# Optimization experiments

Measured on AMD Instinct MI355X. Metric: run time of the kernel, lower is better.

The kernel has to match this reference:

```python
import jax, jax.numpy as jnp
import numpy as np


def squash(t, axis=-1):
    sq = jnp.sum(t * t, axis=axis, keepdims=True)
    scale = sq / (1.0 + sq)
    return scale * t / jnp.sqrt(sq + 1e-8)


def setup_inputs() -> dict:
    key = jax.random.key(0)
    k1, k2 = jax.random.split(key)
    B, in_caps, out_caps, in_dim, out_dim = 128, 2048, 32, 8, 16
    x = jax.random.normal(k1, (B, in_caps, in_dim), dtype=jnp.float32)
    W = jax.random.normal(k2, (in_caps, out_caps, in_dim, out_dim), dtype=jnp.float32)
    return {"x": x, "W": W}


def reference(x, W):
    # x: [B, in_caps, in_dim], W: [in_caps, out_caps, in_dim, out_dim]
    # u_hat: [B, in_caps, out_caps, out_dim]
    u_hat = jnp.einsum('bni,noid->bnod', x, W)
    B, in_caps, out_caps, _ = u_hat.shape
    b = jnp.zeros((B, in_caps, out_caps, 1), dtype=u_hat.dtype)
    v = None
    for i in range(3):
        c = jax.nn.softmax(b, axis=2)              # over out_caps
        s = jnp.sum(c * u_hat, axis=1)             # [B, out_caps, out_dim]
        v = squash(s)                              # [B, out_caps, out_dim]
        if i < 2:
            b = b + jnp.sum(u_hat * v[:, None], axis=-1, keepdims=True)
    return v
```

## Files before the change

### kernel.cpp

```cpp
#include <hip/hip_runtime.h>


constexpr int NC = 2048;
constexpr int OC = 32;
constexpr int OD = 16;

typedef const __attribute__((address_space(1))) void* gas1_t;
typedef __attribute__((address_space(3))) void* las3_t;

__device__ __forceinline__ void gld16(const void* g, void* l) {
    __builtin_amdgcn_global_load_lds((gas1_t)g, (las3_t)l, 16, 0, 0);
}

#define MEMFENCE() asm volatile("" ::: "memory")
#define BAR() do { MEMFENCE(); __builtin_amdgcn_s_barrier(); MEMFENCE(); } while (0)

template<int NR, bool FIRST, bool ATOMIC>
__global__ __launch_bounds__(256)
void caps_pass(const float* __restrict__ xg, const float* __restrict__ Wg,
               const float* __restrict__ vin, float* __restrict__ pout)
{
    __shared__ float4 Wl[2][1024];

    constexpr int NSUPC = 2048 / NR;
    const int tid  = threadIdx.x;
    const int bid  = blockIdx.x;
    const int bt   = bid / NSUPC;
    const int nsup = bid % NSUPC;
    const int w    = __builtin_amdgcn_readfirstlane(tid >> 6);
    const int lane = tid & 63;
    const int o    = lane & 31;
    const int h    = lane >> 5;
    const int sw   = o & 7;
    const int b0   = bt * 16 + w * 4;
    const int nbase = nsup * NR;

    const float4* Wg4 = (const float4*)Wg;

    float4 acc[4][2];
#pragma unroll
    for (int r = 0; r < 4; ++r)
#pragma unroll
        for (int qq = 0; qq < 2; ++qq) acc[r][qq] = make_float4(0.f, 0.f, 0.f, 0.f);

    float4 vr[4][2];
    if (!FIRST) {
        const float4* v4 = (const float4*)vin;
#pragma unroll
        for (int r = 0; r < 4; ++r)
#pragma unroll
            for (int qq = 0; qq < 2; ++qq)
                vr[r][qq] = v4[(size_t)(b0 + r) * 128 + o * 4 + h * 2 + qq];
    }

#pragma unroll
    for (int j = 0; j < 4; ++j) {
        const int L = tid + 256 * j;
        const int oo = L >> 5, cc = L & 31;
        gld16(&Wg4[(size_t)nbase * 1024 + oo * 32 + (cc ^ (oo & 7))], &Wl[0][L]);
    }

#pragma unroll 1
    for (int t = 0; t < NR; ++t) {
        BAR();
        if (t + 1 < NR) {
#pragma unroll
            for (int j = 0; j < 4; ++j) {
                const int L = tid + 256 * j;
                const int oo = L >> 5, cc = L & 31;
                gld16(&Wg4[(size_t)(nbase + t + 1) * 1024 + oo * 32 + (cc ^ (oo & 7))],
                      &Wl[(t + 1) & 1][L]);
            }
            asm volatile("s_waitcnt vmcnt(4)" ::: "memory");
        } else {
            asm volatile("s_waitcnt vmcnt(0)" ::: "memory");
        }
        BAR();

        const int n = nbase + t;
        float xs[4][8];
#pragma unroll
        for (int r = 0; r < 4; ++r) {
            const float* xp = xg + ((size_t)(b0 + r) * NC + n) * 8;
#pragma unroll
            for (int i = 0; i < 8; ++i) xs[r][i] = xp[i];
        }
        const float4* wrow = &Wl[t & 1][o * 32];

        __builtin_amdgcn_s_setprio(1);
        if (FIRST) {
#pragma unroll
            for (int i = 0; i < 8; ++i)
#pragma unroll
                for (int qq = 0; qq < 2; ++qq) {
                    const float4 wv = wrow[(i * 4 + h * 2 + qq) ^ sw];
#pragma unroll
                    for (int r = 0; r < 4; ++r) {
                        acc[r][qq].x = fmaf(xs[r][i], wv.x, acc[r][qq].x);
                        acc[r][qq].y = fmaf(xs[r][i], wv.y, acc[r][qq].y);
                        acc[r][qq].z = fmaf(xs[r][i], wv.z, acc[r][qq].z);
                        acc[r][qq].w = fmaf(xs[r][i], wv.w, acc[r][qq].w);
                    }
                }
        } else {
            float4 u[4][2];
#pragma unroll
            for (int r = 0; r < 4; ++r)
#pragma unroll
                for (int qq = 0; qq < 2; ++qq) u[r][qq] = make_float4(0.f, 0.f, 0.f, 0.f);
#pragma unroll
            for (int i = 0; i < 8; ++i)
#pragma unroll
                for (int qq = 0; qq < 2; ++qq) {
                    const float4 wv = wrow[(i * 4 + h * 2 + qq) ^ sw];
#pragma unroll
                    for (int r = 0; r < 4; ++r) {
                        u[r][qq].x = fmaf(xs[r][i], wv.x, u[r][qq].x);
                        u[r][qq].y = fmaf(xs[r][i], wv.y, u[r][qq].y);
                        u[r][qq].z = fmaf(xs[r][i], wv.z, u[r][qq].z);
                        u[r][qq].w = fmaf(xs[r][i], wv.w, u[r][qq].w);
                    }
                }
#pragma unroll
            for (int r = 0; r < 4; ++r) {
                float tp = 0.f;
#pragma unroll
                for (int qq = 0; qq < 2; ++qq) {
                    tp = fmaf(u[r][qq].x, vr[r][qq].x, tp);
                    tp = fmaf(u[r][qq].y, vr[r][qq].y, tp);
                    tp = fmaf(u[r][qq].z, vr[r][qq].z, tp);
                    tp = fmaf(u[r][qq].w, vr[r][qq].w, tp);
                }
                const float tt = tp + __shfl_xor(tp, 32);
                const float e = __expf(tt);
                float Z = e;
                Z += __shfl_xor(Z, 1);
                Z += __shfl_xor(Z, 2);
                Z += __shfl_xor(Z, 4);
                Z += __shfl_xor(Z, 8);
                Z += __shfl_xor(Z, 16);
                const float c = e / Z;
#pragma unroll
                for (int qq = 0; qq < 2; ++qq) {
                    acc[r][qq].x = fmaf(c, u[r][qq].x, acc[r][qq].x);
                    acc[r][qq].y = fmaf(c, u[r][qq].y, acc[r][qq].y);
                    acc[r][qq].z = fmaf(c, u[r][qq].z, acc[r][qq].z);
                    acc[r][qq].w = fmaf(c, u[r][qq].w, acc[r][qq].w);
                }
            }
        }
        __builtin_amdgcn_s_setprio(0);
    }

    const float sc = FIRST ? (1.0f / 32.0f) : 1.0f;
    if (ATOMIC) {
#pragma unroll
        for (int r = 0; r < 4; ++r) {
            float* sb = pout + (size_t)(b0 + r) * (OC * OD) + o * OD + h * 8;
#pragma unroll
            for (int qq = 0; qq < 2; ++qq) {
                atomicAdd(sb + qq * 4 + 0, acc[r][qq].x * sc);
                atomicAdd(sb + qq * 4 + 1, acc[r][qq].y * sc);
                atomicAdd(sb + qq * 4 + 2, acc[r][qq].z * sc);
                atomicAdd(sb + qq * 4 + 3, acc[r][qq].w * sc);
            }
        }
    } else {
        float4* P4 = (float4*)pout;
#pragma unroll
        for (int r = 0; r < 4; ++r) {
            const size_t base = ((size_t)(nsup * 128 + b0 + r) * 4 + h * 2) * 32 + o;
#pragma unroll
            for (int qq = 0; qq < 2; ++qq) {
                float4 v;
                v.x = acc[r][qq].x * sc; v.y = acc[r][qq].y * sc;
                v.z = acc[r][qq].z * sc; v.w = acc[r][qq].w * sc;
                P4[base + (size_t)qq * 32] = v;
            }
        }
    }
}

template<int NS>
__global__ void reduce_squash(const float* __restrict__ P, const float* __restrict__ vprev,
                              float* __restrict__ vout)
{
    __shared__ float sqb[256];
    const int tid = threadIdx.x;
    const int blk = blockIdx.x;
    const float4* P4 = (const float4*)P;

    float4 a = make_float4(0.f, 0.f, 0.f, 0.f);
#pragma unroll 8
    for (int ns = 0; ns < NS; ++ns) {
        const float4 p = P4[(size_t)ns * 16384 + blk * 256 + tid];
        a.x += p.x; a.y += p.y; a.z += p.z; a.w += p.w;
    }
    sqb[tid] = a.x * a.x + a.y * a.y + a.z * a.z + a.w * a.w;
    __syncthreads();
    const int base = tid & 0x9F;
    const float sq = sqb[base] + sqb[base + 32] + sqb[base + 64] + sqb[base + 96];
    const float f = sq / ((1.0f + sq) * sqrtf(sq + 1e-8f));

    const int b  = blk * 2 + (tid >> 7);
    const int hq = (tid >> 5) & 3;
    const int o  = tid & 31;
    const size_t unit = (size_t)(b * 32 + o) * 4 + hq;
    float4 r;
    r.x = a.x * f; r.y = a.y * f; r.z = a.z * f; r.w = a.w * f;
    if (vprev) {
        const float4 p = ((const float4*)vprev)[unit];
        r.x += p.x; r.y += p.y; r.z += p.z; r.w += p.w;
    }
    ((float4*)vout)[unit] = r;
}

__global__ void squash_k(const float* __restrict__ s, const float* __restrict__ vprev,
                         float* __restrict__ vout)
{
    const int row = blockIdx.x * blockDim.x + threadIdx.x;
    if (row >= 128 * 32) return;
    const float4* s4 = (const float4*)s;
    float4 t[4];
    float sq = 0.f;
#pragma unroll
    for (int q = 0; q < 4; ++q) {
        t[q] = s4[row * 4 + q];
        sq += t[q].x * t[q].x + t[q].y * t[q].y + t[q].z * t[q].z + t[q].w * t[q].w;
    }
    const float f = sq / ((1.0f + sq) * sqrtf(sq + 1e-8f));
    float4* o4 = (float4*)vout;
#pragma unroll
    for (int q = 0; q < 4; ++q) {
        float4 r;
        r.x = t[q].x * f; r.y = t[q].y * f; r.z = t[q].z * f; r.w = t[q].w * f;
        if (vprev) {
            const float4 p = ((const float4*)vprev)[row * 4 + q];
            r.x += p.x; r.y += p.y; r.z += p.z; r.w += p.w;
        }
        o4[row * 4 + q] = r;
    }
}

extern "C" void kernel_launch(void* const* d_in, const int* in_sizes, int n_in,
                              void* d_out, int out_size, void* d_ws, size_t ws_size,
                              hipStream_t stream)
{
    const float* x = (const float*)d_in[0];
    const float* W = (const float*)d_in[1];
    float* out = (float*)d_out;

    const size_t P1 = (size_t)128 * 128 * 512;
    const size_t P2 = (size_t)64 * 128 * 512;
    const size_t NEED1 = (P1 + 2 * 65536) * sizeof(float);
    const size_t NEED2 = (P2 + 2 * 65536) * sizeof(float);

    if (ws_size >= NEED1) {
        float* P  = (float*)d_ws;
        float* v0 = P + P1;
        float* vs = v0 + 65536;

        caps_pass<16, true, false><<<dim3(1024), dim3(256), 0, stream>>>(x, W, nullptr, P);
        reduce_squash<128><<<dim3(64), dim3(256), 0, stream>>>(P, nullptr, v0);

        caps_pass<16, false, false><<<dim3(1024), dim3(256), 0, stream>>>(x, W, v0, P);
        reduce_squash<128><<<dim3(64), dim3(256), 0, stream>>>(P, v0, vs);

        caps_pass<16, false, false><<<dim3(1024), dim3(256), 0, stream>>>(x, W, vs, P);
        reduce_squash<128><<<dim3(64), dim3(256), 0, stream>>>(P, nullptr, out);
    } else if (ws_size >= NEED2) {
        float* P  = (float*)d_ws;
        float* v0 = P + P2;
        float* vs = v0 + 65536;

        caps_pass<32, true, false><<<dim3(512), dim3(256), 0, stream>>>(x, W, nullptr, P);
        reduce_squash<64><<<dim3(64), dim3(256), 0, stream>>>(P, nullptr, v0);

        caps_pass<32, false, false><<<dim3(512), dim3(256), 0, stream>>>(x, W, v0, P);
        reduce_squash<64><<<dim3(64), dim3(256), 0, stream>>>(P, v0, vs);

        caps_pass<32, false, false><<<dim3(512), dim3(256), 0, stream>>>(x, W, vs, P);
        reduce_squash<64><<<dim3(64), dim3(256), 0, stream>>>(P, nullptr, out);
    } else {
        float* s  = (float*)d_ws;
        float* v0 = s + 65536;
        float* vs = v0 + 65536;
        const size_t sbytes = (size_t)65536 * sizeof(float);

        hipMemsetAsync(s, 0, sbytes, stream);
        caps_pass<16, true, true><<<dim3(1024), dim3(256), 0, stream>>>(x, W, nullptr, s);
        squash_k<<<dim3(16), dim3(256), 0, stream>>>(s, nullptr, v0);

        hipMemsetAsync(s, 0, sbytes, stream);
        caps_pass<16, false, true><<<dim3(1024), dim3(256), 0, stream>>>(x, W, v0, s);
        squash_k<<<dim3(16), dim3(256), 0, stream>>>(s, v0, vs);

        hipMemsetAsync(s, 0, sbytes, stream);
        caps_pass<16, false, true><<<dim3(1024), dim3(256), 0, stream>>>(x, W, vs, s);
        squash_k<<<dim3(16), dim3(256), 0, stream>>>(s, nullptr, out);
    }
}
```

Baseline: 195.5 us.

## Stream W directly from global into registers instead of LDS double-buffering

Removes the LDS double-buffered async global-to-LDS staging of W, along with its barriers and priority hints. Each lane now loads its own W float4s straight from global memory, software-prefetching the next pair of rows into registers. This is meant to eliminate barrier stalls and LDS traffic. In exchange, the four waves that share a W tile each fetch it separately through L1/L2, with no block-level sharing, and the loads are less coalesced.

```diff
diff --git a/kernel.cpp b/kernel.cpp
--- a/kernel.cpp
+++ b/kernel.cpp
@@ -5,34 +5,21 @@
 constexpr int OC = 32;
 constexpr int OD = 16;
 
-typedef const __attribute__((address_space(1))) void* gas1_t;
-typedef __attribute__((address_space(3))) void* las3_t;
-
-__device__ __forceinline__ void gld16(const void* g, void* l) {
-    __builtin_amdgcn_global_load_lds((gas1_t)g, (las3_t)l, 16, 0, 0);
-}
-
-#define MEMFENCE() asm volatile("" ::: "memory")
-#define BAR() do { MEMFENCE(); __builtin_amdgcn_s_barrier(); MEMFENCE(); } while (0)
-
 template<int NR, bool FIRST, bool ATOMIC>
 __global__ __launch_bounds__(256)
-void caps_pass(const float* __restrict__ xg, const float* __restrict__ Wg,
-               const float* __restrict__ vin, float* __restrict__ pout)
-{
-    __shared__ float4 Wl[2][1024];
-
+void caps_stream(const float* __restrict__ xg, const float* __restrict__ Wg,
+                 const float* __restrict__ vin, float* __restrict__ pout)
+{
     constexpr int NSUPC = 2048 / NR;
     const int tid  = threadIdx.x;
     const int bid  = blockIdx.x;
-    const int bt   = bid / NSUPC;
     const int nsup = bid % NSUPC;
+    const int bq   = bid / NSUPC;
     const int w    = __builtin_amdgcn_readfirstlane(tid >> 6);
     const int lane = tid & 63;
     const int o    = lane & 31;
     const int h    = lane >> 5;
-    const int sw   = o & 7;
-    const int b0   = bt * 16 + w * 4;
+    const int b0   = (bq * 4 + w) * 4;
     const int nbase = nsup * NR;
 
     const float4* Wg4 = (const float4*)Wg;
@@ -53,31 +40,10 @@
                 vr[r][qq] = v4[(size_t)(b0 + r) * 128 + o * 4 + h * 2 + qq];
     }
 
-#pragma unroll
-    for (int j = 0; j < 4; ++j) {
-        const int L = tid + 256 * j;
-        const int oo = L >> 5, cc = L & 31;
-        gld16(&Wg4[(size_t)nbase * 1024 + oo * 32 + (cc ^ (oo & 7))], &Wl[0][L]);
-    }
-
 #pragma unroll 1
     for (int t = 0; t < NR; ++t) {
-        BAR();
-        if (t + 1 < NR) {
-#pragma unroll
-            for (int j = 0; j < 4; ++j) {
-                const int L = tid + 256 * j;
-                const int oo = L >> 5, cc = L & 31;
-                gld16(&Wg4[(size_t)(nbase + t + 1) * 1024 + oo * 32 + (cc ^ (oo & 7))],
-                      &Wl[(t + 1) & 1][L]);
-            }
-            asm volatile("s_waitcnt vmcnt(4)" ::: "memory");
-        } else {
-            asm volatile("s_waitcnt vmcnt(0)" ::: "memory");
-        }
-        BAR();
-
         const int n = nbase + t;
+
         float xs[4][8];
 #pragma unroll
         for (int r = 0; r < 4; ++r) {
@@ -85,42 +51,53 @@
 #pragma unroll
             for (int i = 0; i < 8; ++i) xs[r][i] = xp[i];
         }
-        const float4* wrow = &Wl[t & 1][o * 32];
-
-        __builtin_amdgcn_s_setprio(1);
-        if (FIRST) {
-#pragma unroll
-            for (int i = 0; i < 8; ++i)
+
+        const float4* wn = Wg4 + (size_t)n * 1024 + o * 32 + h * 2;
+
+        float4 u[4][2];
+#pragma unroll
+        for (int r = 0; r < 4; ++r)
+#pragma unroll
+            for (int qq = 0; qq < 2; ++qq) u[r][qq] = make_float4(0.f, 0.f, 0.f, 0.f);
+
+        float4 wA[2][2], wB[2][2];
+#pragma unroll
+        for (int j = 0; j < 2; ++j)
+#pragma unroll
+            for (int qq = 0; qq < 2; ++qq) wA[j][qq] = wn[j * 4 + qq];
+
+#pragma unroll
+        for (int ip = 0; ip < 4; ++ip) {
+            if (ip < 3) {
+#pragma unroll
+                for (int j = 0; j < 2; ++j)
+#pragma unroll
+                    for (int qq = 0; qq < 2; ++qq)
+                        wB[j][qq] = wn[(ip * 2 + 2 + j) * 4 + qq];
+            }
+#pragma unroll
+            for (int j = 0; j < 2; ++j) {
+                const int i = ip * 2 + j;
 #pragma unroll
                 for (int qq = 0; qq < 2; ++qq) {
-                    const float4 wv = wrow[(i * 4 + h * 2 + qq) ^ sw];
+                    const float4 wv = wA[j][qq];
 #pragma unroll
                     for (int r = 0; r < 4; ++r) {
-                        acc[r][qq].x = fmaf(xs[r][i], wv.x, acc[r][qq].x);
-                        acc[r][qq].y = fmaf(xs[r][i], wv.y, acc[r][qq].y);
-                        acc[r][qq].z = fmaf(xs[r][i], wv.z, acc[r][qq].z);
-                        acc[r][qq].w = fmaf(xs[r][i], wv.w, acc[r][qq].w);
+                        float4* dst = FIRST ? &acc[r][qq] : &u[r][qq];
+                        dst->x = fmaf(xs[r][i], wv.x, dst->x);
+                        dst->y = fmaf(xs[r][i], wv.y, dst->y);
+                        dst->z = fmaf(xs[r][i], wv.z, dst->z);
+                        dst->w = fmaf(xs[r][i], wv.w, dst->w);
                     }
                 }
-        } else {
-            float4 u[4][2];
-#pragma unroll
-            for (int r = 0; r < 4; ++r)
-#pragma unroll
-                for (int qq = 0; qq < 2; ++qq) u[r][qq] = make_float4(0.f, 0.f, 0.f, 0.f);
-#pragma unroll
-            for (int i = 0; i < 8; ++i)
-#pragma unroll
-                for (int qq = 0; qq < 2; ++qq) {
-                    const float4 wv = wrow[(i * 4 + h * 2 + qq) ^ sw];
-#pragma unroll
-                    for (int r = 0; r < 4; ++r) {
-                        u[r][qq].x = fmaf(xs[r][i], wv.x, u[r][qq].x);
-                        u[r][qq].y = fmaf(xs[r][i], wv.y, u[r][qq].y);
-                        u[r][qq].z = fmaf(xs[r][i], wv.z, u[r][qq].z);
-                        u[r][qq].w = fmaf(xs[r][i], wv.w, u[r][qq].w);
-                    }
-                }
+            }
+#pragma unroll
+            for (int j = 0; j < 2; ++j)
+#pragma unroll
+                for (int qq = 0; qq < 2; ++qq) wA[j][qq] = wB[j][qq];
+        }
+
+        if (!FIRST) {
 #pragma unroll
             for (int r = 0; r < 4; ++r) {
                 float tp = 0.f;
@@ -149,7 +126,6 @@
                 }
             }
         }
-        __builtin_amdgcn_s_setprio(0);
     }
 
     const float sc = FIRST ? (1.0f / 32.0f) : 1.0f;
@@ -260,26 +236,26 @@
         float* v0 = P + P1;
         float* vs = v0 + 65536;
 
-        caps_pass<16, true, false><<<dim3(1024), dim3(256), 0, stream>>>(x, W, nullptr, P);
+        caps_stream<16, true, false><<<dim3(1024), dim3(256), 0, stream>>>(x, W, nullptr, P);
         reduce_squash<128><<<dim3(64), dim3(256), 0, stream>>>(P, nullptr, v0);
 
-        caps_pass<16, false, false><<<dim3(1024), dim3(256), 0, stream>>>(x, W, v0, P);
+        caps_stream<16, false, false><<<dim3(1024), dim3(256), 0, stream>>>(x, W, v0, P);
         reduce_squash<128><<<dim3(64), dim3(256), 0, stream>>>(P, v0, vs);
 
-        caps_pass<16, false, false><<<dim3(1024), dim3(256), 0, stream>>>(x, W, vs, P);
+        caps_stream<16, false, false><<<dim3(1024), dim3(256), 0, stream>>>(x, W, vs, P);
         reduce_squash<128><<<dim3(64), dim3(256), 0, stream>>>(P, nullptr, out);
     } else if (ws_size >= NEED2) {
         float* P  = (float*)d_ws;
         float* v0 = P + P2;
         float* vs = v0 + 65536;
 
-        caps_pass<32, true, false><<<dim3(512), dim3(256), 0, stream>>>(x, W, nullptr, P);
+        caps_stream<32, true, false><<<dim3(512), dim3(256), 0, stream>>>(x, W, nullptr, P);
         reduce_squash<64><<<dim3(64), dim3(256), 0, stream>>>(P, nullptr, v0);
 
-        caps_pass<32, false, false><<<dim3(512), dim3(256), 0, stream>>>(x, W, v0, P);
+        caps_stream<32, false, false><<<dim3(512), dim3(256), 0, stream>>>(x, W, v0, P);
         reduce_squash<64><<<dim3(64), dim3(256), 0, stream>>>(P, v0, vs);
 
-        caps_pass<32, false, false><<<dim3(512), dim3(256), 0, stream>>>(x, W, vs, P);
+        caps_stream<32, false, false><<<dim3(512), dim3(256), 0, stream>>>(x, W, vs, P);
         reduce_squash<64><<<dim3(64), dim3(256), 0, stream>>>(P, nullptr, out);
     } else {
         float* s  = (float*)d_ws;
@@ -288,15 +264,15 @@
         const size_t sbytes = (size_t)65536 * sizeof(float);
 
         hipMemsetAsync(s, 0, sbytes, stream);
-        caps_pass<16, true, true><<<dim3(1024), dim3(256), 0, stream>>>(x, W, nullptr, s);
+        caps_stream<16, true, true><<<dim3(1024), dim3(256), 0, stream>>>(x, W, nullptr, s);
         squash_k<<<dim3(16), dim3(256), 0, stream>>>(s, nullptr, v0);
 
         hipMemsetAsync(s, 0, sbytes, stream);
-        caps_pass<16, false, true><<<dim3(1024), dim3(256), 0, stream>>>(x, W, v0, s);
+        caps_stream<16, false, true><<<dim3(1024), dim3(256), 0, stream>>>(x, W, v0, s);
         squash_k<<<dim3(16), dim3(256), 0, stream>>>(s, v0, vs);
 
         hipMemsetAsync(s, 0, sbytes, stream);
-        caps_pass<16, false, true><<<dim3(1024), dim3(256), 0, stream>>>(x, W, vs, s);
+        caps_stream<16, false, true><<<dim3(1024), dim3(256), 0, stream>>>(x, W, vs, s);
         squash_k<<<dim3(16), dim3(256), 0, stream>>>(s, nullptr, out);
     }
 }
```

Measured after the change: 388.0 us. +98.5%, slower.

## Pre-transpose W and stream it from registers in a new 8-row caps kernel

Applied to the files above, without the earlier changes.

Adds a kernel that transposes W once into a coalesced layout in workspace. A new caps_stream8 kernel then streams W straight from global memory into registers with software double-buffering, replacing the LDS-staged path. Each wave handles 8 batch rows per W load, and the grid shrinks to 512 blocks. The cost is an extra pass that reads and writes the 32MB W, more workspace, and heavy register pressure from the 8x8 x tile and the accumulators.

```diff
diff --git a/kernel.cpp b/kernel.cpp
--- a/kernel.cpp
+++ b/kernel.cpp
@@ -14,6 +14,161 @@
 
 #define MEMFENCE() asm volatile("" ::: "memory")
 #define BAR() do { MEMFENCE(); __builtin_amdgcn_s_barrier(); MEMFENCE(); } while (0)
+
+__global__ __launch_bounds__(256)
+void transpose_W(const float* __restrict__ Wg, float* __restrict__ Wtg)
+{
+    const float4* W4  = (const float4*)Wg;
+    float4* Wt4 = (float4*)Wtg;
+    const int n = blockIdx.x;
+    const int tid = threadIdx.x;
+#pragma unroll
+    for (int j = 0; j < 4; ++j) {
+        const int L  = j * 256 + tid;
+        const int o  = L & 31;
+        const int dq = (L >> 5) & 3;
+        const int i  = L >> 7;
+        Wt4[(size_t)n * 1024 + L] = W4[(size_t)n * 1024 + o * 32 + i * 4 + dq];
+    }
+}
+
+template<bool FIRST>
+__global__ __launch_bounds__(256)
+void caps_stream8(const float* __restrict__ xg, const float* __restrict__ Wtg,
+                  const float* __restrict__ vin, float* __restrict__ pout)
+{
+    const int tid  = threadIdx.x;
+    const int bid  = blockIdx.x;
+    const int bt   = bid >> 7;
+    const int nsup = bid & 127;
+    const int w    = __builtin_amdgcn_readfirstlane(tid >> 6);
+    const int lane = tid & 63;
+    const int o    = lane & 31;
+    const int h    = lane >> 5;
+    const int b0   = bt * 32 + w * 8;
+    const int nbase = nsup * 16;
+
+    const float4* Wt4 = (const float4*)Wtg;
+
+    float4 acc[8][2];
+#pragma unroll
+    for (int r = 0; r < 8; ++r)
+#pragma unroll
+        for (int qq = 0; qq < 2; ++qq) acc[r][qq] = make_float4(0.f, 0.f, 0.f, 0.f);
+
+    float4 vr[8][2];
+    if (!FIRST) {
+        const float4* v4 = (const float4*)vin;
+#pragma unroll
+        for (int r = 0; r < 8; ++r)
+#pragma unroll
+            for (int qq = 0; qq < 2; ++qq)
+                vr[r][qq] = v4[(size_t)(b0 + r) * 128 + o * 4 + h * 2 + qq];
+    }
+
+#pragma unroll 1
+    for (int t = 0; t < 16; ++t) {
+        const int n = nbase + t;
+
+        float xs[8][8];
+        {
+            const float* xb = xg + ((size_t)b0 * NC + n) * 8;
+#pragma unroll
+            for (int r = 0; r < 8; ++r)
+#pragma unroll
+                for (int i = 0; i < 8; ++i) xs[r][i] = xb[(size_t)r * NC * 8 + i];
+        }
+
+        const float4* wn = Wt4 + (size_t)n * 1024 + h * 64 + o;
+
+        float4 u[8][2];
+#pragma unroll
+        for (int r = 0; r < 8; ++r)
+#pragma unroll
+            for (int qq = 0; qq < 2; ++qq) u[r][qq] = make_float4(0.f, 0.f, 0.f, 0.f);
+
+        float4 wA[2][2], wB[2][2];
+#pragma unroll
+        for (int j = 0; j < 2; ++j)
+#pragma unroll
+            for (int qq = 0; qq < 2; ++qq) wA[j][qq] = wn[j * 128 + qq * 32];
+
+#pragma unroll
+        for (int ip = 0; ip < 4; ++ip) {
+            if (ip < 3) {
+#pragma unroll
+                for (int j = 0; j < 2; ++j)
+#pragma unroll
+                    for (int qq = 0; qq < 2; ++qq)
+                        wB[j][qq] = wn[(ip * 2 + 2 + j) * 128 + qq * 32];
+            }
+#pragma unroll
+            for (int j = 0; j < 2; ++j) {
+                const int i = ip * 2 + j;
+#pragma unroll
+                for (int qq = 0; qq < 2; ++qq) {
+                    const float4 wv = wA[j][qq];
+#pragma unroll
+                    for (int r = 0; r < 8; ++r) {
+                        float4* dst = FIRST ? &acc[r][qq] : &u[r][qq];
+                        dst->x = fmaf(xs[r][i], wv.x, dst->x);
+                        dst->y = fmaf(xs[r][i], wv.y, dst->y);
+                        dst->z = fmaf(xs[r][i], wv.z, dst->z);
+                        dst->w = fmaf(xs[r][i], wv.w, dst->w);
+                    }
+                }
+            }
+#pragma unroll
+            for (int j = 0; j < 2; ++j)
+#pragma unroll
+                for (int qq = 0; qq < 2; ++qq) wA[j][qq] = wB[j][qq];
+        }
+
+        if (!FIRST) {
+#pragma unroll
+            for (int r = 0; r < 8; ++r) {
+                float tp = 0.f;
+#pragma unroll
+                for (int qq = 0; qq < 2; ++qq) {
+                    tp = fmaf(u[r][qq].x, vr[r][qq].x, tp);
+                    tp = fmaf(u[r][qq].y, vr[r][qq].y, tp);
+                    tp = fmaf(u[r][qq].z, vr[r][qq].z, tp);
+                    tp = fmaf(u[r][qq].w, vr[r][qq].w, tp);
+                }
+                const float tt = tp + __shfl_xor(tp, 32);
+                const float e = __expf(tt);
+                float Z = e;
+                Z += __shfl_xor(Z, 1);
+                Z += __shfl_xor(Z, 2);
+                Z += __shfl_xor(Z, 4);
+                Z += __shfl_xor(Z, 8);
+                Z += __shfl_xor(Z, 16);
+                const float c = e / Z;
+#pragma unroll
+                for (int qq = 0; qq < 2; ++qq) {
+                    acc[r][qq].x = fmaf(c, u[r][qq].x, acc[r][qq].x);
+                    acc[r][qq].y = fmaf(c, u[r][qq].y, acc[r][qq].y);
+                    acc[r][qq].z = fmaf(c, u[r][qq].z, acc[r][qq].z);
+                    acc[r][qq].w = fmaf(c, u[r][qq].w, acc[r][qq].w);
+                }
+            }
+        }
+    }
+
+    const float sc = FIRST ? (1.0f / 32.0f) : 1.0f;
+    float4* P4 = (float4*)pout;
+#pragma unroll
+    for (int r = 0; r < 8; ++r) {
+        const size_t base = ((size_t)(nsup * 128 + b0 + r) * 4 + h * 2) * 32 + o;
+#pragma unroll
+        for (int qq = 0; qq < 2; ++qq) {
+            float4 v;
+            v.x = acc[r][qq].x * sc; v.y = acc[r][qq].y * sc;
+            v.z = acc[r][qq].z * sc; v.w = acc[r][qq].w * sc;
+            P4[base + (size_t)qq * 32] = v;
+        }
+    }
+}
 
 template<int NR, bool FIRST, bool ATOMIC>
 __global__ __launch_bounds__(256)
@@ -250,12 +405,28 @@
     const float* W = (const float*)d_in[1];
     float* out = (float*)d_out;
 
+    const size_t WT = (size_t)2048 * 32 * 128;
     const size_t P1 = (size_t)128 * 128 * 512;
-    const size_t P2 = (size_t)64 * 128 * 512;
-    const size_t NEED1 = (P1 + 2 * 65536) * sizeof(float);
-    const size_t NEED2 = (P2 + 2 * 65536) * sizeof(float);
+    const size_t NEED1 = (WT + P1 + 2 * 65536) * sizeof(float);
+    const size_t NEED2 = (P1 + 2 * 65536) * sizeof(float);
 
     if (ws_size >= NEED1) {
+        float* Wt = (float*)d_ws;
+        float* P  = Wt + WT;
+        float* v0 = P + P1;
+        float* vs = v0 + 65536;
+
+        transpose_W<<<dim3(2048), dim3(256), 0, stream>>>(W, Wt);
+
+        caps_stream8<true><<<dim3(512), dim3(256), 0, stream>>>(x, Wt, nullptr, P);
+        reduce_squash<128><<<dim3(64), dim3(256), 0, stream>>>(P, nullptr, v0);
+
+        caps_stream8<false><<<dim3(512), dim3(256), 0, stream>>>(x, Wt, v0, P);
+        reduce_squash<128><<<dim3(64), dim3(256), 0, stream>>>(P, v0, vs);
+
+        caps_stream8<false><<<dim3(512), dim3(256), 0, stream>>>(x, Wt, vs, P);
+        reduce_squash<128><<<dim3(64), dim3(256), 0, stream>>>(P, nullptr, out);
+    } else if (ws_size >= NEED2) {
         float* P  = (float*)d_ws;
         float* v0 = P + P1;
         float* vs = v0 + 65536;
@@ -268,19 +439,6 @@
 
         caps_pass<16, false, false><<<dim3(1024), dim3(256), 0, stream>>>(x, W, vs, P);
         reduce_squash<128><<<dim3(64), dim3(256), 0, stream>>>(P, nullptr, out);
-    } else if (ws_size >= NEED2) {
-        float* P  = (float*)d_ws;
-        float* v0 = P + P2;
-        float* vs = v0 + 65536;
-
-        caps_pass<32, true, false><<<dim3(512), dim3(256), 0, stream>>>(x, W, nullptr, P);
-        reduce_squash<64><<<dim3(64), dim3(256), 0, stream>>>(P, nullptr, v0);
-
-        caps_pass<32, false, false><<<dim3(512), dim3(256), 0, stream>>>(x, W, v0, P);
-        reduce_squash<64><<<dim3(64), dim3(256), 0, stream>>>(P, v0, vs);
-
-        caps_pass<32, false, false><<<dim3(512), dim3(256), 0, stream>>>(x, W, vs, P);
-        reduce_squash<64><<<dim3(64), dim3(256), 0, stream>>>(P, nullptr, out);
     } else {
         float* s  = (float*)d_ws;
         float* v0 = s + 65536;
```

New measurement: 227.1 us. +16.2%, slower.
